# Optimization experiments

Hardware: AMD Instinct MI355X
Metric: run time of the kernel (lower is better)

Reference implementation:

```python
import jax, jax.numpy as jnp
import numpy as np

N_E = 8192
E_DIM = 256
BETA = 0.25


def setup_inputs() -> dict:
    key = jax.random.key(0)
    k1, k2 = jax.random.split(key)
    z = jax.random.normal(k1, (16, E_DIM, 32, 32), dtype=jnp.float32)
    # nn.Embedding init: uniform(-1/n_e, 1/n_e)
    e_w = jax.random.uniform(k2, (N_E, E_DIM), dtype=jnp.float32,
                             minval=-1.0 / N_E, maxval=1.0 / N_E)
    return {"z": z, "e_w": e_w}


def reference(z, e_w):
    B, C, H, W = z.shape  # C == e_dim
    n_e = e_w.shape[0]
    # (B,C,H,W) -> (N, D)
    z_flat = jnp.transpose(z, (0, 2, 3, 1)).reshape(-1, C)
    # squared euclidean distances: ||z||^2 + ||e||^2 - 2 z.e  -> (N, n_e)
    z_sq = jnp.sum(z_flat * z_flat, axis=1, keepdims=True)
    e_sq = jnp.sum(e_w * e_w, axis=1)
    distances = z_sq + e_sq[None, :] - 2.0 * (z_flat @ e_w.T)
    indices = jnp.argmin(distances, axis=1)  # (N,)
    one_hot = jax.nn.one_hot(indices, n_e, dtype=z.dtype)  # (N, n_e)
    # one_hot @ e_w == gather
    z_q_flat = e_w[indices]
    z_q = jnp.transpose(z_q_flat.reshape(B, H, W, C), (0, 3, 1, 2))
    sg = jax.lax.stop_gradient
    loss_embed = jnp.mean((sg(z_q) - z) ** 2)
    loss_commit = jnp.mean((z_q - sg(z)) ** 2)
    loss = loss_embed + BETA * loss_commit
    # straight-through estimator
    z_q_st = z + sg(z_q - z)
    avg_probs = jnp.mean(one_hot, axis=0)
    perplexity = jnp.exp(-jnp.sum(avg_probs * jnp.log(avg_probs + 1e-10)))
    return loss, z_q_st, perplexity, one_hot, indices
```

## Files before the change

### kernel.cpp

```cpp
#include <hip/hip_runtime.h>
#include <hip/hip_bf16.h>
#include <math.h>

#define N_ROWS 16384
#define DIM    256
#define NE     8192
#define QMARGIN 21

#define SOFF 4194308
#define Z_HEAD 12083202ULL
#define Z4_BASE 12083204ULL
#define N4_TOTAL 31582207ULL
#define C4_PER_BLK 30843ULL
#define Z_TAIL 138412032ULL

typedef __bf16 bf16x8 __attribute__((ext_vector_type(8)));
typedef float  f32x4  __attribute__((ext_vector_type(4)));
typedef float  vf4    __attribute__((ext_vector_type(4)));

__device__ __forceinline__ void gload_lds16(const __bf16* g, __bf16* l) {
  __builtin_amdgcn_global_load_lds(
      (const __attribute__((address_space(1))) unsigned int*)g,
      (__attribute__((address_space(3))) unsigned int*)l, 16, 0, 0);
}

__global__ void k_prep(const float* __restrict__ z, float* __restrict__ zf,
                       __bf16* __restrict__ zfb) {
  __shared__ float tile[32][33];
  int ct = blockIdx.x, ht = blockIdx.y, b = blockIdx.z;
  int tx = threadIdx.x & 31, ty = threadIdx.x >> 5;
  int c0 = ct * 32, hw0 = ht * 32;
  const size_t zb = (size_t)b * 256 * 1024;
#pragma unroll
  for (int p = 0; p < 4; ++p) {
    int c = p * 8 + ty;
    tile[c][tx] = z[zb + (size_t)(c0 + c) * 1024 + hw0 + tx];
  }
  __syncthreads();
#pragma unroll
  for (int p = 0; p < 4; ++p) {
    int r = p * 8 + ty;
    zf[(size_t)(b * 1024 + hw0 + r) * DIM + c0 + tx] = tile[tx][r];
  }
  if (threadIdx.x < 128) {
    int r = threadIdx.x >> 2, kc = threadIdx.x & 3;
    int row = b * 1024 + hw0 + r;
    bf16x8 v;
#pragma unroll
    for (int j = 0; j < 8; ++j) v[j] = (__bf16)tile[kc * 8 + j][r];
    int tn = row >> 7, g = (row >> 4) & 7, m15 = row & 15, kt = c0 >> 5;
    *(bf16x8*)(zfb + (size_t)tn * 32768 + kt * 4096 + g * 512 + (kc * 16 + m15) * 8) = v;
  }
}

__global__ void k_cvt_e(const float* __restrict__ ew, __bf16* __restrict__ ewb) {
  int gid = blockIdx.x * 256 + threadIdx.x;
  int r = gid >> 5, kc8 = gid & 31;
  const float* s = ew + (size_t)r * DIM + kc8 * 8;
  float4 v0 = *(const float4*)s, v1 = *(const float4*)(s + 4);
  bf16x8 v = {(__bf16)v0.x, (__bf16)v0.y, (__bf16)v0.z, (__bf16)v0.w,
              (__bf16)v1.x, (__bf16)v1.y, (__bf16)v1.z, (__bf16)v1.w};
  int t = r >> 7, g = (r >> 4) & 7, m15 = r & 15, kt = kc8 >> 2, kc = kc8 & 3;
  *(bf16x8*)(ewb + (size_t)t * 32768 + kt * 4096 + g * 512 + (kc * 16 + m15) * 8) = v;
}

__global__ __launch_bounds__(256, 2) void k_score(const __bf16* __restrict__ zfb,
                                                  const __bf16* __restrict__ ewb,
                                                  int2* __restrict__ part2,
                                                  float* __restrict__ oz) {
  __shared__ __align__(16) __bf16 Afull[32768];
  __shared__ __align__(16) __bf16 Bs[2][4096];
  const int tid = threadIdx.x;
  const int lane = tid & 63, wave = tid >> 6;
  const int wm = wave >> 1, wn = wave & 1;
  const int quad = lane >> 4, l15 = lane & 15;
  const int bx = blockIdx.x, byc = blockIdx.y;
  const int bid = byc * 128 + bx;
  const __bf16* Ag = zfb + (size_t)bx * 32768;
  const __bf16* Bg = ewb + (size_t)byc * 262144;
  const size_t blk4 = (size_t)bid * C4_PER_BLK;
  f32x4* zdst = (f32x4*)(oz + Z4_BASE);
  const f32x4 zero4 = {0.f, 0.f, 0.f, 0.f};

  if (bid == 0 && tid == 0) {
    __builtin_nontemporal_store(0.f, oz + Z_HEAD);
    __builtin_nontemporal_store(0.f, oz + Z_HEAD + 1);
    __builtin_nontemporal_store(0.f, oz + Z_TAIL);
    __builtin_nontemporal_store(0.f, oz + Z_TAIL + 1);
  }

  {
    const int base = wave * 8192;
#pragma unroll
    for (int i = 0; i < 16; ++i)
      gload_lds16(Ag + base + i * 512 + lane * 8, Afull + base + i * 512);
  }
  {
    const int boff = wave * 1024;
    gload_lds16(Bg + boff + lane * 8, Bs[0] + boff);
    gload_lds16(Bg + boff + 512 + lane * 8, Bs[0] + boff + 512);
  }

  f32x4 acc[4][4];
#pragma unroll
  for (int i = 0; i < 4; ++i)
#pragma unroll
    for (int j = 0; j < 4; ++j) acc[i][j] = (f32x4){0.f, 0.f, 0.f, 0.f};
  int r1[16], r2[16];
#pragma unroll
  for (int i = 0; i < 16; ++i) { r1[i] = 0x7fffffff; r2[i] = 0x7fffffff; }

  for (int it = 0; it < 64; ++it) {
    const int bt = it >> 3, kt = it & 7, buf = it & 1;
    __syncthreads();
    if (it < 63) {
      const int nx = it + 1;
      const __bf16* src = Bg + (nx >> 3) * 32768 + (nx & 7) * 4096 + wave * 1024;
      gload_lds16(src + lane * 8, Bs[buf ^ 1] + wave * 1024);
      gload_lds16(src + 512 + lane * 8, Bs[buf ^ 1] + wave * 1024 + 512);
    }
    if (it <= 60) {
#pragma unroll
      for (int s = 0; s < 2; ++s) {
        size_t slot = (size_t)(it * 2 + s) * 256 + tid;
        if (slot < C4_PER_BLK) {
          size_t g4 = blk4 + slot;
          if (g4 < N4_TOTAL) __builtin_nontemporal_store(zero4, zdst + g4);
        }
      }
    }
    bf16x8 af[4], bfr[4];
#pragma unroll
    for (int mi = 0; mi < 4; ++mi)
      af[mi] = *(const bf16x8*)(Afull + kt * 4096 + (wm * 4 + mi) * 512 + lane * 8);
#pragma unroll
    for (int ni = 0; ni < 4; ++ni)
      bfr[ni] = *(const bf16x8*)(Bs[buf] + (wn * 4 + ni) * 512 + lane * 8);
#pragma unroll
    for (int mi = 0; mi < 4; ++mi)
#pragma unroll
      for (int ni = 0; ni < 4; ++ni)
        acc[mi][ni] = __builtin_amdgcn_mfma_f32_16x16x32_bf16(af[mi], bfr[ni],
                                                              acc[mi][ni], 0, 0, 0);
    if (kt == 7) {
      const int colb = byc * 1024 + bt * 128 + wn * 64;
#pragma unroll
      for (int mi = 0; mi < 4; ++mi) {
#pragma unroll
        for (int rg = 0; rg < 4; ++rg) {
          const int idx = mi * 4 + rg;
          float s0 = -2.f * acc[mi][0][rg], s1 = -2.f * acc[mi][1][rg];
          float s2 = -2.f * acc[mi][2][rg], s3 = -2.f * acc[mi][3][rg];
          int q0 = min(max((int)((s0 + 1.0f) * 131072.0f), 0), 262143);
          int q1 = min(max((int)((s1 + 1.0f) * 131072.0f), 0), 262143);
          int q2 = min(max((int)((s2 + 1.0f) * 131072.0f), 0), 262143);
          int q3 = min(max((int)((s3 + 1.0f) * 131072.0f), 0), 262143);
          int k0 = (q0 << 13) | (colb + l15);
          int k1 = (q1 << 13) | (colb + 16 + l15);
          int k2 = (q2 << 13) | (colb + 32 + l15);
          int k3 = (q3 << 13) | (colb + 48 + l15);
          int a = min(k0, k1), bb = max(k0, k1);
          int c = min(k2, k3), dd = max(k2, k3);
          int t1 = min(a, c);
          int t2 = min(max(a, c), min(bb, dd));
          int n1 = min(r1[idx], t1);
          int n2 = min(max(r1[idx], t1), min(r2[idx], t2));
          r1[idx] = n1; r2[idx] = n2;
        }
      }
#pragma unroll
      for (int i = 0; i < 4; ++i)
#pragma unroll
        for (int j = 0; j < 4; ++j) acc[i][j] = (f32x4){0.f, 0.f, 0.f, 0.f};
    }
  }

#pragma unroll
  for (int mi = 0; mi < 4; ++mi) {
#pragma unroll
    for (int rg = 0; rg < 4; ++rg) {
      const int idx = mi * 4 + rg;
      int k1 = r1[idx], k2 = r2[idx];
#pragma unroll
      for (int d = 1; d < 16; d <<= 1) {
        int o1 = __shfl_xor(k1, d), o2 = __shfl_xor(k2, d);
        k2 = min(max(k1, o1), min(k2, o2));
        k1 = min(k1, o1);
      }
      if (l15 == 0) {
        int row = bx * 128 + wm * 64 + mi * 16 + quad * 4 + rg;
        int2 v; v.x = k1; v.y = k2;
        part2[row * 16 + byc * 2 + wn] = v;
      }
    }
  }
}

__device__ __forceinline__ float np_sumsq_128(const float* __restrict__ p) {
  float r[8];
#pragma unroll
  for (int j = 0; j < 8; ++j) r[j] = __fmul_rn(p[j], p[j]);
  for (int i = 8; i < 128; i += 8) {
#pragma unroll
    for (int j = 0; j < 8; ++j) r[j] = __fadd_rn(r[j], __fmul_rn(p[i + j], p[i + j]));
  }
  return __fadd_rn(__fadd_rn(__fadd_rn(r[0], r[1]), __fadd_rn(r[2], r[3])),
                   __fadd_rn(__fadd_rn(r[4], r[5]), __fadd_rn(r[6], r[7])));
}

__global__ __launch_bounds__(256) void k_pick(const int2* __restrict__ part2,
                                              const float* __restrict__ zf,
                                              const float* __restrict__ ew,
                                              float* __restrict__ idxF,
                                              float* __restrict__ losspart) {
  __shared__ int cand[4][40];
  __shared__ int cnts[4];
  const int t = threadIdx.x, lane = t & 63, wv = t >> 6;
  const int row = blockIdx.x * 4 + wv;
  if (lane == 0) cnts[wv] = 0;
  int2 pv;
  if (lane < 16) pv = part2[row * 16 + lane];
  else { pv.x = 0x7fffffff; pv.y = 0x7fffffff; }
  int kmin = pv.x;
#pragma unroll
  for (int d = 1; d < 64; d <<= 1) kmin = min(kmin, __shfl_xor(kmin, d));
  const int qthr = min((kmin >> 13) + QMARGIN, 262143);
  const int kthr = (qthr << 13) | 8191;
  __syncthreads();
  if (lane < 16) {
    if (pv.x <= kthr) { int p = atomicAdd(&cnts[wv], 1); cand[wv][p] = pv.x & 8191; }
    if (pv.y <= kthr) { int p = atomicAdd(&cnts[wv], 1); cand[wv][p] = pv.y & 8191; }
  }
  __syncthreads();
  const int cnt = cnts[wv];
  const float* zr = zf + (size_t)row * DIM;
  float bd = INFINITY; int bj = 0x7fffffff;
  if (lane < cnt) {
    int j = cand[wv][lane];
    const float* e = ew + (size_t)j * DIM;
    float acc = 0.f;
    for (int k = 0; k < DIM; ++k) acc = __builtin_fmaf(zr[k], e[k], acc);
    float esq = __fadd_rn(np_sumsq_128(e), np_sumsq_128(e + 128));
    float zsq = __fadd_rn(np_sumsq_128(zr), np_sumsq_128(zr + 128));
    bd = __fsub_rn(__fadd_rn(zsq, esq), __fmul_rn(2.0f, acc));
    bj = j;
  }
#pragma unroll
  for (int d = 1; d < 64; d <<= 1) {
    float od = __shfl_xor(bd, d); int oj = __shfl_xor(bj, d);
    if (od < bd || (od == bd && oj < bj)) { bd = od; bj = oj; }
  }
  int c = lane * 4;
  float4 e4 = *reinterpret_cast<const float4*>(ew + (size_t)bj * DIM + c);
  float4 z4 = *reinterpret_cast<const float4*>(zr + c);
  float t0 = __fsub_rn(e4.x, z4.x), t1 = __fsub_rn(e4.y, z4.y);
  float t2 = __fsub_rn(e4.z, z4.z), t3 = __fsub_rn(e4.w, z4.w);
  float s = __fadd_rn(__fadd_rn(__fmul_rn(t0, t0), __fmul_rn(t1, t1)),
                      __fadd_rn(__fmul_rn(t2, t2), __fmul_rn(t3, t3)));
#pragma unroll
  for (int d = 1; d < 64; d <<= 1) s += __shfl_xor(s, d);
  if (lane == 0) {
    idxF[row] = (float)bj;
    losspart[row] = s;
  }
}

__global__ __launch_bounds__(256) void k_scalars(const float* __restrict__ idxF,
                                                 const float* __restrict__ losspart,
                                                 float* __restrict__ out) {
  __shared__ int hist[NE];
  __shared__ float red[256];
  int t = threadIdx.x;
  for (int i = t; i < NE; i += 256) hist[i] = 0;
  __syncthreads();
  float ls = 0.f;
  for (int i = t; i < N_ROWS; i += 256) {
    atomicAdd(&hist[(int)idxF[i]], 1);
    ls += losspart[i];
  }
  __syncthreads();
  float es = 0.f;
  for (int i = t; i < NE; i += 256) {
    float p = (float)hist[i] * (1.0f / 16384.0f);
    es += p * logf(p + 1e-10f);
  }
  red[t] = es; __syncthreads();
  for (int w = 128; w > 0; w >>= 1) { if (t < w) red[t] += red[t + w]; __syncthreads(); }
  float esum = red[0]; __syncthreads();
  red[t] = ls; __syncthreads();
  for (int w = 128; w > 0; w >>= 1) { if (t < w) red[t] += red[t + w]; __syncthreads(); }
  if (t == 0) {
    out[4194305] = expf(-esum);
    float m = red[0] * (1.0f / 4194304.0f);
    out[0] = __fadd_rn(m, __fmul_rn(0.25f, m));
  }
}

__global__ void k_zq_out(const float* __restrict__ z, const float* __restrict__ ew,
                         const float* __restrict__ idxF, float* __restrict__ out) {
  __shared__ float tileE[32][33];
  __shared__ int sidx[32];
  int ct = blockIdx.x, ht = blockIdx.y, b = blockIdx.z;
  int tx = threadIdx.x & 31, ty = threadIdx.x >> 5;
  int c0 = ct * 32, hw0 = ht * 32;
  if (threadIdx.x < 32) sidx[threadIdx.x] = (int)idxF[b * 1024 + hw0 + threadIdx.x];
  __syncthreads();
#pragma unroll
  for (int p = 0; p < 4; ++p) {
    int r = p * 8 + ty;
    tileE[tx][r] = ew[(size_t)sidx[r] * DIM + c0 + tx];
  }
  __syncthreads();
  float* outq = out + 1;
#pragma unroll
  for (int p = 0; p < 4; ++p) {
    int cl = p * 8 + ty;
    size_t gi = (size_t)(b * 256 + c0 + cl) * 1024 + hw0 + tx;
    float zv = z[gi];
    outq[gi] = __fadd_rn(zv, __fsub_rn(tileE[cl][tx], zv));
  }
}

__global__ void k_onehot(const float* __restrict__ idxF, float* __restrict__ out) {
  int bx = blockIdx.x;
  int t = threadIdx.x;
  if (bx < 963) {
    int row = bx;
    int idx = (int)idxF[row];
    float* p = out + 4194306 + (size_t)row * NE;
    if (t == 0) {
      float2 h; h.x = (0 == idx) ? 1.f : 0.f; h.y = (1 == idx) ? 1.f : 0.f;
      *(float2*)p = h;
      float2 q; q.x = (8190 == idx) ? 1.f : 0.f; q.y = (8191 == idx) ? 1.f : 0.f;
      *(float2*)(p + 8190) = q;
    }
    vf4* b4 = (vf4*)(p + 2);
#pragma unroll
    for (int it = 0; it < 8; ++it) {
      int i = it * 256 + t;
      if (i < 2047) {
        int c = 2 + i * 4;
        vf4 v;
        v.x = (c     == idx) ? 1.f : 0.f;
        v.y = (c + 1 == idx) ? 1.f : 0.f;
        v.z = (c + 2 == idx) ? 1.f : 0.f;
        v.w = (c + 3 == idx) ? 1.f : 0.f;
        __builtin_nontemporal_store(v, b4 + i);
      }
    }
  } else {
    int row = 963 + (bx - 963) * 256 + t;
    if (row < N_ROWS) {
      int idx = (int)idxF[row];
      out[4194306 + (size_t)row * NE + idx] = 1.0f;
    }
  }
}

extern "C" void kernel_launch(void* const* d_in, const int* in_sizes, int n_in,
                              void* d_out, int out_size, void* d_ws, size_t ws_size,
                              hipStream_t stream) {
  const float* z  = (const float*)d_in[0];
  const float* ew = (const float*)d_in[1];
  float* out = (float*)d_out;
  float*  zf    = out + SOFF;
  __bf16* zfb   = (__bf16*)(out + SOFF + 4194304);
  __bf16* ewb   = (__bf16*)(out + SOFF + 6291456);
  int2*   part2 = (int2*)(out + SOFF + 7340032);
  float*  lprt  = out + SOFF + 7864320;
  float*  idxF  = out + 138412034;

  k_prep<<<dim3(8, 32, 16), 256, 0, stream>>>(z, zf, zfb);
  k_cvt_e<<<dim3(1024), 256, 0, stream>>>(ew, ewb);
  k_score<<<dim3(128, 8), 256, 0, stream>>>(zfb, ewb, part2, out);
  k_pick<<<dim3(4096), 256, 0, stream>>>(part2, zf, ew, idxF, lprt);
  k_scalars<<<1, 256, 0, stream>>>(idxF, lprt, out);
  k_zq_out<<<dim3(8, 32, 16), 256, 0, stream>>>(z, ew, idxF, out);
  k_onehot<<<dim3(1024), 256, 0, stream>>>(idxF, out);
}
```

Before: 828.8 us.

## Fuse codebook conversion into prep and one-hot writes into z_q output kernel

Merges the codebook bf16 conversion into the prep kernel and the one-hot scratch region overwrite into the z_q output kernel, removing two launches. The histogram moves from the single-block scalars kernel to global atomics in the pick kernel, zeroed during prep. The score kernel's scratch zeroing is batched into bursts every eighth iteration, and the pick dot product uses float4 loads. This cuts launch overhead and the serial single-block histogram, at the cost of global atomic contention and more complex index bookkeeping for the scratch regions.

```diff
diff --git a/kernel.cpp b/kernel.cpp
--- a/kernel.cpp
+++ b/kernel.cpp
@@ -8,11 +8,12 @@
 #define QMARGIN 21
 
 #define SOFF 4194308
-#define Z_HEAD 12083202ULL
+#define GHOFF 12075012ULL
 #define Z4_BASE 12083204ULL
 #define N4_TOTAL 31582207ULL
 #define C4_PER_BLK 30843ULL
-#define Z_TAIL 138412032ULL
+#define ZQ4_COUNT 1972223ULL
+#define ZQ4_PER_BLK 482
 
 typedef __bf16 bf16x8 __attribute__((ext_vector_type(8)));
 typedef float  f32x4  __attribute__((ext_vector_type(4)));
@@ -24,8 +25,9 @@
       (__attribute__((address_space(3))) unsigned int*)l, 16, 0, 0);
 }
 
-__global__ void k_prep(const float* __restrict__ z, float* __restrict__ zf,
-                       __bf16* __restrict__ zfb) {
+__global__ void k_prep(const float* __restrict__ z, const float* __restrict__ ew,
+                       float* __restrict__ zf, __bf16* __restrict__ zfb,
+                       __bf16* __restrict__ ewb, int* __restrict__ ghist) {
   __shared__ float tile[32][33];
   int ct = blockIdx.x, ht = blockIdx.y, b = blockIdx.z;
   int tx = threadIdx.x & 31, ty = threadIdx.x >> 5;
@@ -51,17 +53,19 @@
     int tn = row >> 7, g = (row >> 4) & 7, m15 = row & 15, kt = c0 >> 5;
     *(bf16x8*)(zfb + (size_t)tn * 32768 + kt * 4096 + g * 512 + (kc * 16 + m15) * 8) = v;
   }
-}
-
-__global__ void k_cvt_e(const float* __restrict__ ew, __bf16* __restrict__ ewb) {
-  int gid = blockIdx.x * 256 + threadIdx.x;
-  int r = gid >> 5, kc8 = gid & 31;
-  const float* s = ew + (size_t)r * DIM + kc8 * 8;
-  float4 v0 = *(const float4*)s, v1 = *(const float4*)(s + 4);
-  bf16x8 v = {(__bf16)v0.x, (__bf16)v0.y, (__bf16)v0.z, (__bf16)v0.w,
-              (__bf16)v1.x, (__bf16)v1.y, (__bf16)v1.z, (__bf16)v1.w};
-  int t = r >> 7, g = (r >> 4) & 7, m15 = r & 15, kt = kc8 >> 2, kc = kc8 & 3;
-  *(bf16x8*)(ewb + (size_t)t * 32768 + kt * 4096 + g * 512 + (kc * 16 + m15) * 8) = v;
+  const int fid = blockIdx.x + 8 * blockIdx.y + 256 * blockIdx.z;
+  if (fid < 1024) {
+    int gid = fid * 256 + threadIdx.x;
+    int r = gid >> 5, kc8 = gid & 31;
+    const float* s = ew + (size_t)r * DIM + kc8 * 8;
+    float4 v0 = *(const float4*)s, v1 = *(const float4*)(s + 4);
+    bf16x8 v = {(__bf16)v0.x, (__bf16)v0.y, (__bf16)v0.z, (__bf16)v0.w,
+                (__bf16)v1.x, (__bf16)v1.y, (__bf16)v1.z, (__bf16)v1.w};
+    int t = r >> 7, g = (r >> 4) & 7, m15 = r & 15, kt = kc8 >> 2, kc = kc8 & 3;
+    *(bf16x8*)(ewb + (size_t)t * 32768 + kt * 4096 + g * 512 + (kc * 16 + m15) * 8) = v;
+  } else if (fid < 1056) {
+    ghist[(fid - 1024) * 256 + threadIdx.x] = 0;
+  }
 }
 
 __global__ __launch_bounds__(256, 2) void k_score(const __bf16* __restrict__ zfb,
@@ -82,13 +86,6 @@
   f32x4* zdst = (f32x4*)(oz + Z4_BASE);
   const f32x4 zero4 = {0.f, 0.f, 0.f, 0.f};
 
-  if (bid == 0 && tid == 0) {
-    __builtin_nontemporal_store(0.f, oz + Z_HEAD);
-    __builtin_nontemporal_store(0.f, oz + Z_HEAD + 1);
-    __builtin_nontemporal_store(0.f, oz + Z_TAIL);
-    __builtin_nontemporal_store(0.f, oz + Z_TAIL + 1);
-  }
-
   {
     const int base = wave * 8192;
 #pragma unroll
@@ -119,10 +116,11 @@
       gload_lds16(src + lane * 8, Bs[buf ^ 1] + wave * 1024);
       gload_lds16(src + 512 + lane * 8, Bs[buf ^ 1] + wave * 1024 + 512);
     }
-    if (it <= 60) {
-#pragma unroll
-      for (int s = 0; s < 2; ++s) {
-        size_t slot = (size_t)(it * 2 + s) * 256 + tid;
+    if (kt == 0) {
+      const int burst = it >> 3;
+#pragma unroll
+      for (int s = 0; s < 16; ++s) {
+        size_t slot = (size_t)(burst * 16 + s) * 256 + tid;
         if (slot < C4_PER_BLK) {
           size_t g4 = blk4 + slot;
           if (g4 < N4_TOTAL) __builtin_nontemporal_store(zero4, zdst + g4);
@@ -212,7 +210,8 @@
                                               const float* __restrict__ zf,
                                               const float* __restrict__ ew,
                                               float* __restrict__ idxF,
-                                              float* __restrict__ losspart) {
+                                              float* __restrict__ losspart,
+                                              int* __restrict__ ghist) {
   __shared__ int cand[4][40];
   __shared__ int cnts[4];
   const int t = threadIdx.x, lane = t & 63, wv = t >> 6;
@@ -239,7 +238,14 @@
     int j = cand[wv][lane];
     const float* e = ew + (size_t)j * DIM;
     float acc = 0.f;
-    for (int k = 0; k < DIM; ++k) acc = __builtin_fmaf(zr[k], e[k], acc);
+    for (int k = 0; k < DIM; k += 4) {
+      float4 e4 = *(const float4*)(e + k);
+      float4 z4 = *(const float4*)(zr + k);
+      acc = __builtin_fmaf(z4.x, e4.x, acc);
+      acc = __builtin_fmaf(z4.y, e4.y, acc);
+      acc = __builtin_fmaf(z4.z, e4.z, acc);
+      acc = __builtin_fmaf(z4.w, e4.w, acc);
+    }
     float esq = __fadd_rn(np_sumsq_128(e), np_sumsq_128(e + 128));
     float zsq = __fadd_rn(np_sumsq_128(zr), np_sumsq_128(zr + 128));
     bd = __fsub_rn(__fadd_rn(zsq, esq), __fmul_rn(2.0f, acc));
@@ -262,26 +268,20 @@
   if (lane == 0) {
     idxF[row] = (float)bj;
     losspart[row] = s;
-  }
-}
-
-__global__ __launch_bounds__(256) void k_scalars(const float* __restrict__ idxF,
+    atomicAdd(&ghist[bj], 1);
+  }
+}
+
+__global__ __launch_bounds__(256) void k_scalars(const int* __restrict__ ghist,
                                                  const float* __restrict__ losspart,
                                                  float* __restrict__ out) {
-  __shared__ int hist[NE];
   __shared__ float red[256];
   int t = threadIdx.x;
-  for (int i = t; i < NE; i += 256) hist[i] = 0;
-  __syncthreads();
   float ls = 0.f;
-  for (int i = t; i < N_ROWS; i += 256) {
-    atomicAdd(&hist[(int)idxF[i]], 1);
-    ls += losspart[i];
-  }
-  __syncthreads();
+  for (int i = t; i < N_ROWS; i += 256) ls += losspart[i];
   float es = 0.f;
   for (int i = t; i < NE; i += 256) {
-    float p = (float)hist[i] * (1.0f / 16384.0f);
+    float p = (float)ghist[i] * (1.0f / 16384.0f);
     es += p * logf(p + 1e-10f);
   }
   red[t] = es; __syncthreads();
@@ -319,41 +319,52 @@
     float zv = z[gi];
     outq[gi] = __fadd_rn(zv, __fsub_rn(tileE[cl][tx], zv));
   }
-}
-
-__global__ void k_onehot(const float* __restrict__ idxF, float* __restrict__ out) {
-  int bx = blockIdx.x;
-  int t = threadIdx.x;
-  if (bx < 963) {
-    int row = bx;
-    int idx = (int)idxF[row];
-    float* p = out + 4194306 + (size_t)row * NE;
-    if (t == 0) {
-      float2 h; h.x = (0 == idx) ? 1.f : 0.f; h.y = (1 == idx) ? 1.f : 0.f;
-      *(float2*)p = h;
-      float2 q; q.x = (8190 == idx) ? 1.f : 0.f; q.y = (8191 == idx) ? 1.f : 0.f;
-      *(float2*)(p + 8190) = q;
-    }
-    vf4* b4 = (vf4*)(p + 2);
-#pragma unroll
-    for (int it = 0; it < 8; ++it) {
-      int i = it * 256 + t;
-      if (i < 2047) {
-        int c = 2 + i * 4;
-        vf4 v;
-        v.x = (c     == idx) ? 1.f : 0.f;
-        v.y = (c + 1 == idx) ? 1.f : 0.f;
-        v.z = (c + 2 == idx) ? 1.f : 0.f;
-        v.w = (c + 3 == idx) ? 1.f : 0.f;
-        __builtin_nontemporal_store(v, b4 + i);
-      }
-    }
-  } else {
-    int row = 963 + (bx - 963) * 256 + t;
-    if (row < N_ROWS) {
-      int idx = (int)idxF[row];
-      out[4194306 + (size_t)row * NE + idx] = 1.0f;
-    }
+
+  const int fid = blockIdx.x + 8 * blockIdx.y + 256 * blockIdx.z;
+  float* oh = out + 4194306;
+  {
+    f32x4* dst4 = (f32x4*)(out + 4194308);
+#pragma unroll
+    for (int p = 0; p < 2; ++p) {
+      int slot = p * 256 + (int)threadIdx.x;
+      size_t g4 = (size_t)fid * ZQ4_PER_BLK + slot;
+      if (slot < ZQ4_PER_BLK && g4 < ZQ4_COUNT) {
+        size_t rel = g4 * 4 + 2;
+        int ra = (int)(rel >> 13), rb = (int)((rel + 3) >> 13);
+        int ia = (int)idxF[ra];
+        int ib = (ra == rb) ? ia : (int)idxF[rb];
+        f32x4 v;
+#pragma unroll
+        for (int j = 0; j < 4; ++j) {
+          size_t rj = rel + j;
+          int rowj = (int)(rj >> 13), colj = (int)(rj & 8191);
+          int idxj = (rowj == ra) ? ia : ib;
+          v[j] = (colj == idxj) ? 1.f : 0.f;
+        }
+        __builtin_nontemporal_store(v, dst4 + g4);
+      }
+    }
+  }
+  if (threadIdx.x < 4) {
+    int r = fid * 4 + (int)threadIdx.x;
+    if (r >= 963 && r < N_ROWS) {
+      int idx = (int)idxF[r];
+      oh[(size_t)r * NE + idx] = 1.0f;
+    }
+  }
+  if (fid == 0 && threadIdx.x == 4) {
+    int i0 = (int)idxF[0];
+    oh[0] = (i0 == 0) ? 1.f : 0.f;
+    oh[1] = (i0 == 1) ? 1.f : 0.f;
+    int i962 = (int)idxF[962];
+    oh[(size_t)962 * NE + 8190] = (i962 == 8190) ? 1.f : 0.f;
+    oh[(size_t)962 * NE + 8191] = (i962 == 8191) ? 1.f : 0.f;
+    int i963 = (int)idxF[963];
+    oh[(size_t)963 * NE + 0] = (i963 == 0) ? 1.f : 0.f;
+    oh[(size_t)963 * NE + 1] = (i963 == 1) ? 1.f : 0.f;
+    int il = (int)idxF[16383];
+    oh[(size_t)16383 * NE + 8190] = (il == 8190) ? 1.f : 0.f;
+    oh[(size_t)16383 * NE + 8191] = (il == 8191) ? 1.f : 0.f;
   }
 }
 
@@ -368,13 +379,12 @@
   __bf16* ewb   = (__bf16*)(out + SOFF + 6291456);
   int2*   part2 = (int2*)(out + SOFF + 7340032);
   float*  lprt  = out + SOFF + 7864320;
+  int*    ghist = (int*)(out + GHOFF);
   float*  idxF  = out + 138412034;
 
-  k_prep<<<dim3(8, 32, 16), 256, 0, stream>>>(z, zf, zfb);
-  k_cvt_e<<<dim3(1024), 256, 0, stream>>>(ew, ewb);
+  k_prep<<<dim3(8, 32, 16), 256, 0, stream>>>(z, ew, zf, zfb, ewb, ghist);
   k_score<<<dim3(128, 8), 256, 0, stream>>>(zfb, ewb, part2, out);
-  k_pick<<<dim3(4096), 256, 0, stream>>>(part2, zf, ew, idxF, lprt);
-  k_scalars<<<1, 256, 0, stream>>>(idxF, lprt, out);
+  k_pick<<<dim3(4096), 256, 0, stream>>>(part2, zf, ew, idxF, lprt, ghist);
+  k_scalars<<<1, 256, 0, stream>>>(ghist, lprt, out);
   k_zq_out<<<dim3(8, 32, 16), 256, 0, stream>>>(z, ew, idxF, out);
-  k_onehot<<<dim3(1024), 256, 0, stream>>>(idxF, out);
-}
+}
```

Result: slower. 848.4 us (+2.4%).
